# Optimization experiments

Measured on AMD Instinct MI355X. Metric: run time of the kernel, lower is better.

Reference implementation:

```python
import jax, jax.numpy as jnp
import numpy as np

FIELDS = 32
EMBED = 64
PAIRS = FIELDS * (FIELDS - 1) // 2  # 496
BATCH = 2048


def setup_inputs() -> dict:
    key = jax.random.key(0)
    k1, k2 = jax.random.split(key)
    x = jax.random.normal(k1, (BATCH, FIELDS, EMBED), dtype=jnp.float32)
    kernel = jax.random.normal(k2, (EMBED, PAIRS, EMBED), dtype=jnp.float32) * 0.05
    return {"x": x, "kernel": kernel}


def reference(x, kernel):
    # Pair enumeration (i<j) matching the python double loop order.
    iu, ju = jnp.triu_indices(FIELDS, k=1)
    p = x[:, iu, :]  # (B, P, E)
    q = x[:, ju, :]  # (B, P, E)
    # Original: kp[b,f,pr] = sum_e p[b,pr,e]*kernel[f,pr,e];
    # result[b,pr] = sum_f kp[b,f,pr]*q[b,pr,f]
    # => bilinear form per pair, fused as a single einsum.
    result = jnp.einsum('bpe,fpe,bpf->bp', p, kernel, q)
    return result
```

## Files before the change

kernel.cpp:

```cpp
#include <hip/hip_runtime.h>


constexpr int BATCH  = 2048;
constexpr int FIELDS = 32;
constexpr int EMBED  = 64;
constexpr int PAIRS  = FIELDS * (FIELDS - 1) / 2;

typedef __attribute__((ext_vector_type(8))) short  short8;
typedef __attribute__((ext_vector_type(4))) float  f32x4;

constexpr size_t XN      = (size_t)BATCH * FIELDS * EMBED;
constexpr size_t KPN     = (size_t)PAIRS * 2 * 4 * 64 * 8;
constexpr size_t XH_OFF  = 0;
constexpr size_t XL_OFF  = XH_OFF + XN * 2;
constexpr size_t KPH_OFF = XL_OFF + XN * 2;
constexpr size_t KPL_OFF = KPH_OFF + KPN * 2;
constexpr size_t WS_NEED = KPL_OFF + KPN * 2;

constexpr int XSPLIT_BLOCKS = (int)(XN / 4 / 256);
constexpr int KPACK_BLOCKS  = (int)(PAIRS * 512 / 256);

__device__ __forceinline__ unsigned short bf16_rne(float f) {
    unsigned int u = __float_as_uint(f);
    u = u + 0x7fffu + ((u >> 16) & 1u);
    return (unsigned short)(u >> 16);
}

__global__ __launch_bounds__(256) void prep_kernel(
    const float* __restrict__ x,
    const float* __restrict__ kern,
    unsigned short* __restrict__ xh,
    unsigned short* __restrict__ xl,
    unsigned short* __restrict__ kph,
    unsigned short* __restrict__ kpl)
{
    const int bid = (int)blockIdx.x;
    const int tid = (int)threadIdx.x;

    if (bid < XSPLIT_BLOCKS) {
        const int idx = bid * 256 + tid;
        const float4 v = ((const float4*)x)[idx];
        const float vv[4] = {v.x, v.y, v.z, v.w};
        unsigned short h[4], l[4];
        #pragma unroll
        for (int j = 0; j < 4; ++j) {
            const unsigned int u = __float_as_uint(vv[j]);
            h[j] = (unsigned short)(u >> 16);
            l[j] = bf16_rne(vv[j] - __uint_as_float(u & 0xffff0000u));
        }
        ((ushort4*)xh)[idx] = make_ushort4(h[0], h[1], h[2], h[3]);
        ((ushort4*)xl)[idx] = make_ushort4(l[0], l[1], l[2], l[3]);
    } else {
        const int t    = (bid - XSPLIT_BLOCKS) * 256 + tid;
        const int lane = t & 63;
        const int nc   = (t >> 6) & 3;
        const int ks   = (t >> 8) & 1;
        const int pair = t >> 9;
        const int e    = nc * 16 + (lane & 15);
        const int f0   = ks * 32 + (lane >> 4) * 8;

        short8 h8, l8;
        #pragma unroll
        for (int jj = 0; jj < 8; ++jj) {
            const float v = kern[((size_t)(f0 + jj) * PAIRS + pair) * EMBED + e];
            const unsigned int u = __float_as_uint(v);
            h8[jj] = (short)(u >> 16);
            l8[jj] = (short)bf16_rne(v - __uint_as_float(u & 0xffff0000u));
        }
        *(short8*)(kph + (size_t)t * 8) = h8;
        *(short8*)(kpl + (size_t)t * 8) = l8;
    }
}

__global__ __launch_bounds__(256, 3) void opn_mfma_kernel(
    const float* __restrict__ x,
    const unsigned short* __restrict__ xh,
    const unsigned short* __restrict__ xl,
    const unsigned short* __restrict__ kph,
    const unsigned short* __restrict__ kpl,
    float* __restrict__ out)
{
    const int bid  = (int)blockIdx.x;
    const int p    = bid >> 4;
    const int mt   = bid & 15;
    const int wave = (int)threadIdx.x >> 6;
    const int lane = (int)threadIdx.x & 63;
    const int Mb   = mt * 128 + wave * 32;
    const int g    = lane >> 4;
    const int c    = lane & 15;

    int i = 0, rem = p;
    while (rem >= FIELDS - 1 - i) { rem -= FIELDS - 1 - i; ++i; }
    const int jf = i + 1 + rem;

    f32x4 acc[2][4];
    #pragma unroll
    for (int mr = 0; mr < 2; ++mr)
        #pragma unroll
        for (int nc = 0; nc < 4; ++nc)
            acc[mr][nc] = (f32x4){0.f, 0.f, 0.f, 0.f};

    #pragma unroll
    for (int ks = 0; ks < 2; ++ks) {
        short8 ah[2], al[2];
        #pragma unroll
        for (int mr = 0; mr < 2; ++mr) {
            const int row = Mb + mr * 16 + c;
            const size_t off = ((size_t)row * FIELDS + jf) * EMBED + ks * 32 + g * 8;
            ah[mr] = *(const short8*)(xh + off);
            al[mr] = *(const short8*)(xl + off);
        }
        short8 bh[4], bl[4];
        #pragma unroll
        for (int nc = 0; nc < 4; ++nc) {
            const size_t kidx = (((size_t)(p * 2 + ks) * 4 + nc) * 64 + lane) * 8;
            bh[nc] = *(const short8*)(kph + kidx);
            bl[nc] = *(const short8*)(kpl + kidx);
        }
        #pragma unroll
        for (int mr = 0; mr < 2; ++mr)
            #pragma unroll
            for (int nc = 0; nc < 4; ++nc) {
                acc[mr][nc] = __builtin_amdgcn_mfma_f32_16x16x32_bf16(ah[mr], bh[nc], acc[mr][nc], 0, 0, 0);
                acc[mr][nc] = __builtin_amdgcn_mfma_f32_16x16x32_bf16(ah[mr], bl[nc], acc[mr][nc], 0, 0, 0);
                acc[mr][nc] = __builtin_amdgcn_mfma_f32_16x16x32_bf16(al[mr], bh[nc], acc[mr][nc], 0, 0, 0);
            }
    }

    float z[2][4];
    #pragma unroll
    for (int mr = 0; mr < 2; ++mr)
        #pragma unroll
        for (int t = 0; t < 4; ++t)
            z[mr][t] = 0.f;

    const size_t xi_base = (size_t)i * EMBED + c;
    #pragma unroll
    for (int mr = 0; mr < 2; ++mr)
        #pragma unroll
        for (int t = 0; t < 4; ++t) {
            const int row = Mb + mr * 16 + 4 * g + t;
            const float* xi = x + (size_t)row * (FIELDS * EMBED) + xi_base;
            #pragma unroll
            for (int nc = 0; nc < 4; ++nc)
                z[mr][t] = fmaf(acc[mr][nc][t], xi[nc * 16], z[mr][t]);
        }

    #pragma unroll
    for (int mask = 1; mask < 16; mask <<= 1)
        #pragma unroll
        for (int mr = 0; mr < 2; ++mr)
            #pragma unroll
            for (int t = 0; t < 4; ++t)
                z[mr][t] += __shfl_xor(z[mr][t], mask, 64);

    if (c < 4) {
        const int t = c;
        #pragma unroll
        for (int mr = 0; mr < 2; ++mr) {
            const int row = Mb + mr * 16 + 4 * g + t;
            out[(size_t)row * PAIRS + p] = z[mr][t];
        }
    }
}

__global__ __launch_bounds__(64) void opn_fp32_kernel(
    const float* __restrict__ x,
    const float* __restrict__ kern,
    float* __restrict__ out)
{
    const int bid   = (int)blockIdx.x;
    const int p     = bid >> 5;
    const int btile = bid & 31;
    const int lane  = (int)threadIdx.x;
    const int b     = btile * 64 + lane;

    int i = 0, rem = p;
    while (rem >= FIELDS - 1 - i) { rem -= FIELDS - 1 - i; ++i; }
    const int j = i + 1 + rem;

    const float* xrow_i = x + (size_t)b * (FIELDS * EMBED) + i * EMBED;
    const float* xrow_j = x + (size_t)b * (FIELDS * EMBED) + j * EMBED;
    const float* kp     = kern + (size_t)p * EMBED;

    float acc[EMBED];
    #pragma unroll
    for (int e = 0; e < EMBED; ++e) acc[e] = 0.0f;

    const float4* xj4 = (const float4*)xrow_j;
    #pragma unroll 2
    for (int f4 = 0; f4 < EMBED / 4; ++f4) {
        const float4 v = xj4[f4];
        const float xjf[4] = {v.x, v.y, v.z, v.w};
        #pragma unroll
        for (int s = 0; s < 4; ++s) {
            const float* kf = kp + (size_t)(f4 * 4 + s) * (PAIRS * EMBED);
            #pragma unroll
            for (int e = 0; e < EMBED; ++e)
                acc[e] = fmaf(xjf[s], kf[e], acc[e]);
        }
    }

    float r = 0.0f;
    const float4* xi4 = (const float4*)xrow_i;
    #pragma unroll
    for (int e4 = 0; e4 < EMBED / 4; ++e4) {
        const float4 u = xi4[e4];
        r = fmaf(u.x, acc[e4 * 4 + 0], r);
        r = fmaf(u.y, acc[e4 * 4 + 1], r);
        r = fmaf(u.z, acc[e4 * 4 + 2], r);
        r = fmaf(u.w, acc[e4 * 4 + 3], r);
    }
    out[(size_t)b * PAIRS + p] = r;
}

extern "C" void kernel_launch(void* const* d_in, const int* in_sizes, int n_in,
                              void* d_out, int out_size, void* d_ws, size_t ws_size,
                              hipStream_t stream) {
    const float* x    = (const float*)d_in[0];
    const float* kern = (const float*)d_in[1];
    float*       out  = (float*)d_out;

    if (ws_size < WS_NEED) {
        opn_fp32_kernel<<<dim3(PAIRS * 32), dim3(64), 0, stream>>>(x, kern, out);
        return;
    }

    char* ws = (char*)d_ws;
    unsigned short* xhi = (unsigned short*)(ws + XH_OFF);
    unsigned short* xlo = (unsigned short*)(ws + XL_OFF);
    unsigned short* kph = (unsigned short*)(ws + KPH_OFF);
    unsigned short* kpl = (unsigned short*)(ws + KPL_OFF);

    prep_kernel<<<dim3(XSPLIT_BLOCKS + KPACK_BLOCKS), dim3(256), 0, stream>>>(
        x, kern, xhi, xlo, kph, kpl);
    opn_mfma_kernel<<<dim3(PAIRS * 16), dim3(256), 0, stream>>>(
        x, xhi, xlo, kph, kpl, out);
}
```

Baseline: 127.4 us.

## Stage MFMA operands into LDS via direct global-to-LDS loads with XOR swizzle

```diff
diff --git a/kernel.cpp b/kernel.cpp
--- a/kernel.cpp
+++ b/kernel.cpp
@@ -80,12 +80,16 @@
     const unsigned short* __restrict__ kpl,
     float* __restrict__ out)
 {
+    __shared__ unsigned short smem[24576];
+
     const int bid  = (int)blockIdx.x;
     const int p    = bid >> 4;
     const int mt   = bid & 15;
-    const int wave = (int)threadIdx.x >> 6;
-    const int lane = (int)threadIdx.x & 63;
-    const int Mb   = mt * 128 + wave * 32;
+    const int tid  = (int)threadIdx.x;
+    const int wave = tid >> 6;
+    const int lane = tid & 63;
+    const int Mb0  = mt * 128;
+    const int Mb   = Mb0 + wave * 32;
     const int g    = lane >> 4;
     const int c    = lane & 15;
 
@@ -93,6 +97,30 @@
     while (rem >= FIELDS - 1 - i) { rem -= FIELDS - 1 - i; ++i; }
     const int jf = i + 1 + rem;
 
+    #pragma unroll
+    for (int k = 0; k < 2; ++k) {
+        const int q = tid + 256 * k;
+        unsigned short* ldst_h = &smem[(size_t)(k * 256 + wave * 64) * 8];
+        unsigned short* ldst_l = &smem[4096 + (size_t)(k * 256 + wave * 64) * 8];
+        __builtin_amdgcn_global_load_lds(kph + (size_t)p * 4096 + q * 8, ldst_h, 16, 0, 0);
+        __builtin_amdgcn_global_load_lds(kpl + (size_t)p * 4096 + q * 8, ldst_l, 16, 0, 0);
+    }
+
+    #pragma unroll
+    for (int k = 0; k < 4; ++k) {
+        const int q   = tid + 256 * k;
+        const int row = q >> 3;
+        const int cs  = (q & 7) ^ (row & 7);
+        const size_t goff = ((size_t)(Mb0 + row) * FIELDS + jf) * EMBED + cs * 8;
+        unsigned short* ldst_h = &smem[8192  + (size_t)(k * 256 + wave * 64) * 8];
+        unsigned short* ldst_l = &smem[16384 + (size_t)(k * 256 + wave * 64) * 8];
+        __builtin_amdgcn_global_load_lds(xh + goff, ldst_h, 16, 0, 0);
+        __builtin_amdgcn_global_load_lds(xl + goff, ldst_l, 16, 0, 0);
+    }
+
+    asm volatile("s_waitcnt vmcnt(0)" ::: "memory");
+    __syncthreads();
+
     f32x4 acc[2][4];
     #pragma unroll
     for (int mr = 0; mr < 2; ++mr)
@@ -105,17 +133,17 @@
         short8 ah[2], al[2];
         #pragma unroll
         for (int mr = 0; mr < 2; ++mr) {
-            const int row = Mb + mr * 16 + c;
-            const size_t off = ((size_t)row * FIELDS + jf) * EMBED + ks * 32 + g * 8;
-            ah[mr] = *(const short8*)(xh + off);
-            al[mr] = *(const short8*)(xl + off);
+            const int rl = wave * 32 + mr * 16 + c;
+            const int ch = rl * 8 + ((ks * 4 + g) ^ (rl & 7));
+            ah[mr] = *(const short8*)&smem[8192  + (size_t)ch * 8];
+            al[mr] = *(const short8*)&smem[16384 + (size_t)ch * 8];
         }
         short8 bh[4], bl[4];
         #pragma unroll
         for (int nc = 0; nc < 4; ++nc) {
-            const size_t kidx = (((size_t)(p * 2 + ks) * 4 + nc) * 64 + lane) * 8;
-            bh[nc] = *(const short8*)(kph + kidx);
-            bl[nc] = *(const short8*)(kpl + kidx);
+            const int off = ((ks * 4 + nc) * 64 + lane) * 8;
+            bh[nc] = *(const short8*)&smem[off];
+            bl[nc] = *(const short8*)&smem[4096 + off];
         }
         #pragma unroll
         for (int mr = 0; mr < 2; ++mr)
```

Result: faster. 114.0 us (-10.5%).
